# Kernel optimization log

Measured on AMD Instinct MI355X. Metric: run time of the kernel, lower is better.

The kernel has to match this reference:

```python
import jax, jax.numpy as jnp
import numpy as np

B, N, M = 2, 4096, 4096
QUERY_DIM = 1024
CONTEXT_DIM = 1024
HEADS = 16
DIM_HEAD = 64
INNER = HEADS * DIM_HEAD


def setup_inputs() -> dict:
    key = jax.random.key(0)
    ks = jax.random.split(key, 7)
    s = 0.02
    return {
        "x": jax.random.normal(ks[0], (B, N, QUERY_DIM), dtype=jnp.float32),
        "context": jax.random.normal(ks[1], (B, M, CONTEXT_DIM), dtype=jnp.float32),
        "Wq": jax.random.normal(ks[2], (QUERY_DIM, INNER), dtype=jnp.float32) * s,
        "Wk": jax.random.normal(ks[3], (CONTEXT_DIM, INNER), dtype=jnp.float32) * s,
        "Wv": jax.random.normal(ks[4], (CONTEXT_DIM, INNER), dtype=jnp.float32) * s,
        "Wo": jax.random.normal(ks[5], (INNER, QUERY_DIM), dtype=jnp.float32) * s,
        "bo": jnp.zeros((QUERY_DIM,), dtype=jnp.float32),
    }


def reference(x, context, Wq, Wk, Wv, Wo, bo):
    scale = DIM_HEAD ** -0.5
    # projections, then split heads: b n (h d) -> b h n d
    q = (x @ Wq).reshape(B, N, HEADS, DIM_HEAD).transpose(0, 2, 1, 3)
    k = (context @ Wk).reshape(B, M, HEADS, DIM_HEAD).transpose(0, 2, 1, 3)
    v = (context @ Wv).reshape(B, M, HEADS, DIM_HEAD).transpose(0, 2, 1, 3)
    attn = jnp.einsum('bhnd,bhmd->bhnm', q, k) * scale  # [B,H,N,M]
    attn = jax.nn.softmax(attn, axis=-1)
    out = jnp.einsum('bhnm,bhmd->bhnd', attn, v)
    out = out.transpose(0, 2, 1, 3).reshape(B, N, INNER)  # b h n d -> b n (h d)
    return out @ Wo + bo  # dropout(p=0) is identity
```

## Files before the change

kernel.cpp:

```cpp
#include <hip/hip_runtime.h>

using f16    = _Float16;
using f16x2  = __attribute__((ext_vector_type(2))) _Float16;
using f16x4  = __attribute__((ext_vector_type(4))) _Float16;
using f16x8  = __attribute__((ext_vector_type(8))) _Float16;
using h16x2  = __attribute__((ext_vector_type(2))) __fp16;
using f32x4  = __attribute__((ext_vector_type(4))) float;
using f32x16 = __attribute__((ext_vector_type(16))) float;
using u32    = unsigned int;
using u32x4  = __attribute__((ext_vector_type(4))) u32;

#define DI __device__ __forceinline__

DI f16x4 pack4(float a, float b, float c, float d) {
  f16x2 lo = __builtin_bit_cast(f16x2, __builtin_amdgcn_cvt_pkrtz(a, b));
  f16x2 hi = __builtin_bit_cast(f16x2, __builtin_amdgcn_cvt_pkrtz(c, d));
  f16x4 r; r[0] = lo[0]; r[1] = lo[1]; r[2] = hi[0]; r[3] = hi[1];
  return r;
}

DI u32 pk32(float a, float b) {
  return __builtin_bit_cast(u32, __builtin_amdgcn_cvt_pkrtz(a, b));
}

DI float dot1(u32 wrd, float acc) {
#if __has_builtin(__builtin_amdgcn_fdot2)
  h16x2 one; one[0] = (__fp16)1.f; one[1] = (__fp16)1.f;
  return __builtin_amdgcn_fdot2(__builtin_bit_cast(h16x2, wrd), one, acc, false);
#else
  f16x2 p = __builtin_bit_cast(f16x2, wrd);
  return acc + (float)p[0] + (float)p[1];
#endif
}

DI void gll16(const void* g, void* l) {
  __builtin_amdgcn_global_load_lds((const __attribute__((address_space(1))) u32*)g,
                                   (__attribute__((address_space(3))) u32*)l, 16, 0, 0);
}

DI f16x8 ldfrag(const void* base, int row, int u4) {
  int phys = u4 ^ (row & 7);
  return *(const f16x8*)((const char*)base + row * 128 + phys * 16);
}

DI f32x4 mfma16(f16x8 a, f16x8 b, f32x4 c) {
  return __builtin_amdgcn_mfma_f32_16x16x32_f16(a, b, c, 0, 0, 0);
}
DI f32x16 mfma32(f16x8 a, f16x8 b, f32x16 c) {
  return __builtin_amdgcn_mfma_f32_32x32x16_f16(a, b, c, 0, 0, 0);
}

__global__ void k_cvt2(const float* __restrict__ x, const float* __restrict__ ctx,
                       f16* __restrict__ dst, int n4) {
  int z = blockIdx.y;
  const float* s = z ? ctx : x;
  f16* d = dst + (size_t)z * 8192 * 1024;
  int i = blockIdx.x * blockDim.x + threadIdx.x;
  if (i < n4) {
    float4 v = ((const float4*)s)[i];
    ((f16x4*)d)[i] = pack4(v.x, v.y, v.z, v.w);
  }
}

__global__ void k_wt4(const float* __restrict__ Wq, const float* __restrict__ Wk,
                      const float* __restrict__ Wv, const float* __restrict__ Wo,
                      f16* __restrict__ WTb) {
  int z = blockIdx.z;
  const float* W = z == 0 ? Wq : z == 1 ? Wk : z == 2 ? Wv : Wo;
  f16* WT = WTb + (size_t)z * 1024 * 1024;
  __shared__ float tile[64][65];
  int k0 = blockIdx.y * 64, n0 = blockIdx.x * 64;
  int t = threadIdx.x;
#pragma unroll
  for (int p = 0; p < 4; ++p) {
    int r = p * 16 + (t >> 4);
    int c = (t & 15) * 4;
    float4 v = *(const float4*)&W[(size_t)(k0 + r) * 1024 + n0 + c];
    tile[r][c] = v.x; tile[r][c + 1] = v.y; tile[r][c + 2] = v.z; tile[r][c + 3] = v.w;
  }
  __syncthreads();
#pragma unroll
  for (int p = 0; p < 4; ++p) {
    int n = p * 16 + (t >> 4);
    int k = (t & 15) * 4;
    *(f16x4*)&WT[(size_t)(n0 + n) * 1024 + k0 + k] =
        pack4(tile[k][n], tile[k + 1][n], tile[k + 2][n], tile[k + 3][n]);
  }
}

template <int EPI>
__global__ __launch_bounds__(256) void k_gemm(const f16* __restrict__ A, const f16* __restrict__ Bt,
                                              void* __restrict__ Cp, const float* __restrict__ bias) {
  __shared__ __align__(16) char smem[65536];
  f16* sA = (f16*)smem;
  f16* sB = (f16*)(smem + 32768);
  const int tid = threadIdx.x, w = tid >> 6, lane = tid & 63;
  const int g = lane >> 4, l15 = lane & 15, l7 = lane & 7, l8 = lane >> 3;
  const int m0 = blockIdx.x * 128, n0 = blockIdx.y * 128;
  const int wm = w >> 1, wn = w & 1;
  const int uswz = l7 ^ l8;

  auto stage = [&](int kt, int bufi) {
    int kb = kt * 128;
#pragma unroll
    for (int q = 0; q < 4; ++q) {
      int row = w * 32 + q * 8 + l8;
      gll16((const char*)A + (size_t)(m0 + row) * 2048 + kb + uswz * 16,
            (char*)sA + bufi * 16384 + (w * 32 + q * 8) * 128);
      gll16((const char*)Bt + (size_t)(n0 + row) * 2048 + kb + uswz * 16,
            (char*)sB + bufi * 16384 + (w * 32 + q * 8) * 128);
    }
  };

  f32x4 acc[4][4] = {};
  stage(0, 0);
  for (int kt = 0; kt < 16; ++kt) {
    asm volatile("s_waitcnt vmcnt(0)" ::: "memory");
    __syncthreads();
    if (kt + 1 < 16) stage(kt + 1, (kt + 1) & 1);
    const f16* aL = (const f16*)((const char*)sA + (kt & 1) * 16384);
    const f16* bL = (const f16*)((const char*)sB + (kt & 1) * 16384);
#pragma unroll
    for (int kc = 0; kc < 2; ++kc) {
      f16x8 af[4], bf[4];
#pragma unroll
      for (int mi = 0; mi < 4; ++mi) af[mi] = ldfrag(aL, wm * 64 + mi * 16 + l15, kc * 4 + g);
#pragma unroll
      for (int ni = 0; ni < 4; ++ni) bf[ni] = ldfrag(bL, wn * 64 + ni * 16 + l15, kc * 4 + g);
#pragma unroll
      for (int mi = 0; mi < 4; ++mi)
#pragma unroll
        for (int ni = 0; ni < 4; ++ni) acc[mi][ni] = mfma16(af[mi], bf[ni], acc[mi][ni]);
    }
  }

  if (EPI == 2) {
    float* C = (float*)Cp;
    float bv[4];
#pragma unroll
    for (int ni = 0; ni < 4; ++ni) bv[ni] = bias[n0 + wn * 64 + ni * 16 + l15];
#pragma unroll
    for (int mi = 0; mi < 4; ++mi)
#pragma unroll
      for (int ni = 0; ni < 4; ++ni) {
        int col = n0 + wn * 64 + ni * 16 + l15;
#pragma unroll
        for (int i = 0; i < 4; ++i) {
          int row = m0 + wm * 64 + mi * 16 + g * 4 + i;
          C[(size_t)row * 1024 + col] = acc[mi][ni][i] + bv[ni];
        }
      }
    return;
  }

  __syncthreads();
  f16* Ct = (f16*)smem;
  if (EPI == 0) {
#pragma unroll
    for (int mi = 0; mi < 4; ++mi)
#pragma unroll
      for (int ni = 0; ni < 4; ++ni) {
        int col = wn * 64 + ni * 16 + l15;
#pragma unroll
        for (int i = 0; i < 4; ++i) Ct[(wm * 64 + mi * 16 + g * 4 + i) * 136 + col] = (f16)acc[mi][ni][i];
      }
    __syncthreads();
    f16* C = (f16*)Cp;
#pragma unroll
    for (int p = 0; p < 8; ++p) {
      int r = p * 16 + (tid >> 4), cu = tid & 15;
      f16x8 v = *(const f16x8*)((const char*)Ct + r * 272 + cu * 16);
      *(f16x8*)((char*)C + (size_t)(m0 + r) * 2048 + n0 * 2 + cu * 16) = v;
    }
  } else {
#pragma unroll
    for (int mi = 0; mi < 4; ++mi)
#pragma unroll
      for (int ni = 0; ni < 4; ++ni) {
        int n = wn * 64 + ni * 16 + l15;
        int mcol = wm * 64 + mi * 16 + g * 4;
        *(f16x4*)&Ct[n * 136 + mcol] =
            pack4(acc[mi][ni][0], acc[mi][ni][1], acc[mi][ni][2], acc[mi][ni][3]);
      }
    __syncthreads();
    int b = m0 >> 12, mm = m0 & 4095;
    f16* V = (f16*)Cp;
#pragma unroll
    for (int p = 0; p < 8; ++p) {
      int n = p * 16 + (tid >> 4), cu = tid & 15;
      f16x8 v = *(const f16x8*)((const char*)Ct + n * 272 + cu * 16);
      *(f16x8*)((char*)V + ((size_t)(b * 1024 + n0 + n) * 4096 + mm) * 2 + cu * 16) = v;
    }
  }
}

__global__ __launch_bounds__(256, 2) void k_attn(const f16* __restrict__ Qh, const f16* __restrict__ Kh,
                                                 const f16* __restrict__ VT, f16* __restrict__ Oh) {
  __shared__ __align__(16) char smem[32768];
  const int tid = threadIdx.x, w = tid >> 6, lane = tid & 63;
  const int hi = lane >> 5, c = lane & 31, l7 = lane & 7, l8 = lane >> 3;
  const int bid = blockIdx.x;
  const int bh = (bid & 7) * 4 + (bid >> 7);
  const int qc = (bid >> 3) & 15;
  const int b = bh >> 4, h = bh & 15;
  const int rowB = b * 4096;
  const int qrow0 = rowB + qc * 256 + w * 64;
  const int uswz = l7 ^ l8;

  const f16 ce = (f16)0.18033688f;
  f16x8 bQ0[4], bQ1[4];
#pragma unroll
  for (int ks = 0; ks < 4; ++ks) {
    f16x8 r0 = *(const f16x8*)(Qh + (size_t)(qrow0 + c) * 1024 + h * 64 + ks * 16 + hi * 8);
    f16x8 r1 = *(const f16x8*)(Qh + (size_t)(qrow0 + 32 + c) * 1024 + h * 64 + ks * 16 + hi * 8);
#pragma unroll
    for (int e = 0; e < 8; ++e) { r0[e] *= ce; r1[e] *= ce; }
    bQ0[ks] = r0; bQ1[ks] = r1;
  }

  const f32x16 Z = {};
  f32x16 acc00 = {}, acc01 = {}, acc10 = {}, acc11 = {};
  float lrow0 = 0.f, lrow1 = 0.f;

  auto stage = [&](int t, int bufi) {
    int r = w * 16 + l8;
#pragma unroll
    for (int q = 0; q < 2; ++q) {
      gll16((const char*)Kh + ((size_t)(rowB + t * 64 + r + q * 8) * 1024 + h * 64) * 2 + uswz * 16,
            (char*)smem + bufi * 8192 + (w * 16 + q * 8) * 128);
      gll16((const char*)VT + ((size_t)(b * 1024 + h * 64 + r + q * 8) * 4096 + t * 64) * 2 + uswz * 16,
            (char*)smem + 16384 + bufi * 8192 + (w * 16 + q * 8) * 128);
    }
  };

  auto softpack = [&](f32x16 sA, f32x16 sB, f16x8* bp) -> float {
#pragma unroll
    for (int i = 0; i < 16; ++i) sA[i] = __builtin_amdgcn_exp2f(sA[i]);
#pragma unroll
    for (int i = 0; i < 16; ++i) sB[i] = __builtin_amdgcn_exp2f(sB[i]);
    u32 a[8], d[8];
#pragma unroll
    for (int i = 0; i < 8; ++i) a[i] = pk32(sA[2 * i], sA[2 * i + 1]);
#pragma unroll
    for (int i = 0; i < 8; ++i) d[i] = pk32(sB[2 * i], sB[2 * i + 1]);
    float s0 = 0.f, s1 = 0.f;
#pragma unroll
    for (int i = 0; i < 8; ++i) s0 = dot1(a[i], s0);
#pragma unroll
    for (int i = 0; i < 8; ++i) s1 = dot1(d[i], s1);
    {
      auto s02 = __builtin_amdgcn_permlane32_swap(a[0], a[2], false, false);
      auto s13 = __builtin_amdgcn_permlane32_swap(a[1], a[3], false, false);
      auto s46 = __builtin_amdgcn_permlane32_swap(a[4], a[6], false, false);
      auto s57 = __builtin_amdgcn_permlane32_swap(a[5], a[7], false, false);
      u32x4 w0 = {s02[0], s13[0], s02[1], s13[1]};
      u32x4 w1 = {s46[0], s57[0], s46[1], s57[1]};
      bp[0] = __builtin_bit_cast(f16x8, w0);
      bp[1] = __builtin_bit_cast(f16x8, w1);
    }
    {
      auto s02 = __builtin_amdgcn_permlane32_swap(d[0], d[2], false, false);
      auto s13 = __builtin_amdgcn_permlane32_swap(d[1], d[3], false, false);
      auto s46 = __builtin_amdgcn_permlane32_swap(d[4], d[6], false, false);
      auto s57 = __builtin_amdgcn_permlane32_swap(d[5], d[7], false, false);
      u32x4 w0 = {s02[0], s13[0], s02[1], s13[1]};
      u32x4 w1 = {s46[0], s57[0], s46[1], s57[1]};
      bp[2] = __builtin_bit_cast(f16x8, w0);
      bp[3] = __builtin_bit_cast(f16x8, w1);
    }
    return s0 + s1;
  };

  stage(0, 0);
  for (int t = 0; t < 64; ++t) {
    asm volatile("s_waitcnt vmcnt(0)" ::: "memory");
    __syncthreads();
    if (t + 1 < 64) stage(t + 1, (t + 1) & 1);
    const char* Kl = (const char*)smem + (t & 1) * 8192;
    const char* Vl = (const char*)smem + 16384 + (t & 1) * 8192;

    __builtin_amdgcn_s_setprio(1);
    f16x8 a0 = ldfrag(Kl, c, hi), a1 = ldfrag(Kl, 32 + c, hi);
    f32x16 st00 = mfma32(a0, bQ0[0], Z);
    f32x16 st01 = mfma32(a0, bQ1[0], Z);
    f32x16 st10 = mfma32(a1, bQ0[0], Z);
    f32x16 st11 = mfma32(a1, bQ1[0], Z);
#pragma unroll
    for (int ks = 1; ks < 4; ++ks) {
      a0 = ldfrag(Kl, c, ks * 2 + hi); a1 = ldfrag(Kl, 32 + c, ks * 2 + hi);
      st00 = mfma32(a0, bQ0[ks], st00);
      st01 = mfma32(a0, bQ1[ks], st01);
      st10 = mfma32(a1, bQ0[ks], st10);
      st11 = mfma32(a1, bQ1[ks], st11);
    }
    __builtin_amdgcn_s_setprio(0);

    f16x8 bpA[4], bpB[4];
    lrow0 += softpack(st00, st10, bpA);
    lrow1 += softpack(st01, st11, bpB);

    __builtin_amdgcn_s_setprio(1);
#pragma unroll
    for (int ks = 0; ks < 4; ++ks) {
      f16x8 av0 = ldfrag(Vl, c, ks * 2 + hi);
      f16x8 av1 = ldfrag(Vl, 32 + c, ks * 2 + hi);
      acc00 = mfma32(av0, bpA[ks], acc00);
      acc01 = mfma32(av0, bpB[ks], acc01);
      acc10 = mfma32(av1, bpA[ks], acc10);
      acc11 = mfma32(av1, bpB[ks], acc11);
    }
    __builtin_amdgcn_s_setprio(0);
  }

  float inv0, inv1;
  {
    auto r2 = __builtin_amdgcn_permlane32_swap(__builtin_bit_cast(u32, lrow0),
                                               __builtin_bit_cast(u32, lrow0), false, false);
    inv0 = 1.0f / (__builtin_bit_cast(float, r2[0]) + __builtin_bit_cast(float, r2[1]));
  }
  {
    auto r2 = __builtin_amdgcn_permlane32_swap(__builtin_bit_cast(u32, lrow1),
                                               __builtin_bit_cast(u32, lrow1), false, false);
    inv1 = 1.0f / (__builtin_bit_cast(float, r2[0]) + __builtin_bit_cast(float, r2[1]));
  }

  __syncthreads();
  char* myO = (char*)smem + w * 8192;
#pragma unroll
  for (int rb = 0; rb < 2; ++rb) {
    float iv = rb ? inv1 : inv0;
    int r = rb * 32 + c;
#pragma unroll
    for (int dt = 0; dt < 2; ++dt) {
      const f32x16& A = rb ? (dt ? acc11 : acc01) : (dt ? acc10 : acc00);
#pragma unroll
      for (int q8 = 0; q8 < 4; ++q8) {
        f16x4 hv = pack4(A[q8 * 4] * iv, A[q8 * 4 + 1] * iv, A[q8 * 4 + 2] * iv, A[q8 * 4 + 3] * iv);
        int slot = dt * 4 + q8;
        *(f16x4*)(myO + r * 128 + ((slot ^ (r & 7)) * 16) + hi * 8) = hv;
      }
    }
  }
#pragma unroll
  for (int p = 0; p < 8; ++p) {
    int r = p * 8 + l8;
    f16x8 v = *(const f16x8*)(myO + r * 128 + ((l7 ^ (r & 7)) * 16));
    *(f16x8*)((char*)Oh + ((size_t)(qrow0 + r) * 1024 + h * 64) * 2 + l7 * 16) = v;
  }
}

extern "C" void kernel_launch(void* const* d_in, const int* in_sizes, int n_in,
                              void* d_out, int out_size, void* d_ws, size_t ws_size,
                              hipStream_t stream) {
  const float* x   = (const float*)d_in[0];
  const float* ctx = (const float*)d_in[1];
  const float* Wq  = (const float*)d_in[2];
  const float* Wk  = (const float*)d_in[3];
  const float* Wv  = (const float*)d_in[4];
  const float* Wo  = (const float*)d_in[5];
  const float* bo  = (const float*)d_in[6];
  float* out = (float*)d_out;

  const size_t NR = 8192, KD = 1024;
  if (ws_size < (size_t)(5 * NR * KD * 2 + 4 * KD * KD * 2)) return;

  char* ws = (char*)d_ws;
  f16* xh  = (f16*)ws;
  f16* ch  = xh + NR * KD;
  f16* WqT = ch + NR * KD;
  f16* WkT = WqT + KD * KD;
  f16* WvT = WkT + KD * KD;
  f16* WoT = WvT + KD * KD;
  f16* Qh  = WoT + KD * KD;
  f16* Kh  = Qh + NR * KD;
  f16* VT  = Kh + NR * KD;
  f16* Oh  = xh;

  int n4 = (int)(NR * KD / 4);
  k_cvt2<<<dim3((n4 + 255) / 256, 2), dim3(256), 0, stream>>>(x, ctx, xh, n4);
  k_wt4<<<dim3(16, 16, 4), dim3(256), 0, stream>>>(Wq, Wk, Wv, Wo, WqT);

  dim3 gg(64, 8), gb(256);
  k_gemm<0><<<gg, gb, 0, stream>>>(xh, WqT, (void*)Qh, nullptr);
  k_gemm<0><<<gg, gb, 0, stream>>>(ch, WkT, (void*)Kh, nullptr);
  k_gemm<1><<<gg, gb, 0, stream>>>(ch, WvT, (void*)VT, nullptr);

  k_attn<<<dim3(512), dim3(256), 0, stream>>>(Qh, Kh, VT, Oh);

  k_gemm<2><<<gg, gb, 0, stream>>>(Oh, WoT, (void*)out, bo);
}
```

Measured before the change: 272.4 us.

## Pre-tile K/V into fragment-major layout and shrink attention blocks to two waves

```diff
diff --git a/kernel.cpp b/kernel.cpp
--- a/kernel.cpp
+++ b/kernel.cpp
@@ -41,6 +41,10 @@
 DI f16x8 ldfrag(const void* base, int row, int u4) {
   int phys = u4 ^ (row & 7);
   return *(const f16x8*)((const char*)base + row * 128 + phys * 16);
+}
+
+DI f16x8 ldsc(const void* base, int row, int slot) {
+  return *(const f16x8*)((const char*)base + slot * 1024 + row * 16);
 }
 
 DI f32x4 mfma16(f16x8 a, f16x8 b, f32x4 c) {
@@ -155,7 +159,7 @@
 
   __syncthreads();
   f16* Ct = (f16*)smem;
-  if (EPI == 0) {
+  if (EPI == 0 || EPI == 3) {
 #pragma unroll
     for (int mi = 0; mi < 4; ++mi)
 #pragma unroll
@@ -165,12 +169,25 @@
         for (int i = 0; i < 4; ++i) Ct[(wm * 64 + mi * 16 + g * 4 + i) * 136 + col] = (f16)acc[mi][ni][i];
       }
     __syncthreads();
-    f16* C = (f16*)Cp;
-#pragma unroll
-    for (int p = 0; p < 8; ++p) {
-      int r = p * 16 + (tid >> 4), cu = tid & 15;
-      f16x8 v = *(const f16x8*)((const char*)Ct + r * 272 + cu * 16);
-      *(f16x8*)((char*)C + (size_t)(m0 + r) * 2048 + n0 * 2 + cu * 16) = v;
+    if (EPI == 0) {
+      f16* C = (f16*)Cp;
+#pragma unroll
+      for (int p = 0; p < 8; ++p) {
+        int r = p * 16 + (tid >> 4), cu = tid & 15;
+        f16x8 v = *(const f16x8*)((const char*)Ct + r * 272 + cu * 16);
+        *(f16x8*)((char*)C + (size_t)(m0 + r) * 2048 + n0 * 2 + cu * 16) = v;
+      }
+    } else {
+      int b = m0 >> 12, mmr = m0 & 4095;
+#pragma unroll
+      for (int p = 0; p < 8; ++p) {
+        int r = p * 16 + (tid >> 4), cu = tid & 15;
+        f16x8 v = *(const f16x8*)((const char*)Ct + r * 272 + cu * 16);
+        int kvr = mmr + r;
+        int h = (n0 >> 6) + (cu >> 3);
+        size_t off = ((size_t)((b * 16 + h) * 64 + (kvr >> 6))) * 8192 + (cu & 7) * 1024 + (kvr & 63) * 16;
+        *(f16x8*)((char*)Cp + off) = v;
+      }
     }
   } else {
 #pragma unroll
@@ -184,28 +201,29 @@
       }
     __syncthreads();
     int b = m0 >> 12, mm = m0 & 4095;
-    f16* V = (f16*)Cp;
 #pragma unroll
     for (int p = 0; p < 8; ++p) {
-      int n = p * 16 + (tid >> 4), cu = tid & 15;
-      f16x8 v = *(const f16x8*)((const char*)Ct + n * 272 + cu * 16);
-      *(f16x8*)((char*)V + ((size_t)(b * 1024 + n0 + n) * 4096 + mm) * 2 + cu * 16) = v;
-    }
-  }
-}
-
-__global__ __launch_bounds__(256, 2) void k_attn(const f16* __restrict__ Qh, const f16* __restrict__ Kh,
-                                                 const f16* __restrict__ VT, f16* __restrict__ Oh) {
+      int r = p * 16 + (tid >> 4), cu = tid & 15;
+      f16x8 v = *(const f16x8*)((const char*)Ct + r * 272 + cu * 16);
+      int h = (n0 + r) >> 6, d = (n0 + r) & 63;
+      size_t off = ((size_t)((b * 16 + h) * 64 + (mm >> 6) + (cu >> 3))) * 8192 + (cu & 7) * 1024 + d * 16;
+      *(f16x8*)((char*)Cp + off) = v;
+    }
+  }
+}
+
+__global__ __launch_bounds__(128, 4) void k_attn(const f16* __restrict__ Qh, const f16* __restrict__ Ks,
+                                                 const f16* __restrict__ Vs, f16* __restrict__ Oh) {
   __shared__ __align__(16) char smem[32768];
   const int tid = threadIdx.x, w = tid >> 6, lane = tid & 63;
   const int hi = lane >> 5, c = lane & 31, l7 = lane & 7, l8 = lane >> 3;
   const int bid = blockIdx.x;
-  const int bh = (bid & 7) * 4 + (bid >> 7);
-  const int qc = (bid >> 3) & 15;
+  const int bh = (bid & 7) * 4 + (bid >> 8);
+  const int qc = (bid >> 3) & 31;
   const int b = bh >> 4, h = bh & 15;
   const int rowB = b * 4096;
-  const int qrow0 = rowB + qc * 256 + w * 64;
-  const int uswz = l7 ^ l8;
+  const int qrow0 = rowB + qc * 128 + w * 64;
+  const size_t tb = (size_t)bh * 64 * 8192;
 
   const f16 ce = (f16)0.18033688f;
   f16x8 bQ0[4], bQ1[4];
@@ -223,13 +241,13 @@
   float lrow0 = 0.f, lrow1 = 0.f;
 
   auto stage = [&](int t, int bufi) {
-    int r = w * 16 + l8;
-#pragma unroll
-    for (int q = 0; q < 2; ++q) {
-      gll16((const char*)Kh + ((size_t)(rowB + t * 64 + r + q * 8) * 1024 + h * 64) * 2 + uswz * 16,
-            (char*)smem + bufi * 8192 + (w * 16 + q * 8) * 128);
-      gll16((const char*)VT + ((size_t)(b * 1024 + h * 64 + r + q * 8) * 4096 + t * 64) * 2 + uswz * 16,
-            (char*)smem + 16384 + bufi * 8192 + (w * 16 + q * 8) * 128);
+    const char* bK = (const char*)Ks + tb + (size_t)t * 8192 + lane * 16;
+    const char* bV = (const char*)Vs + tb + (size_t)t * 8192 + lane * 16;
+#pragma unroll
+    for (int q = 0; q < 4; ++q) {
+      int slot = w * 4 + q;
+      gll16(bK + slot * 1024, (char*)smem + bufi * 8192 + slot * 1024);
+      gll16(bV + slot * 1024, (char*)smem + 16384 + bufi * 8192 + slot * 1024);
     }
   };
 
@@ -280,14 +298,14 @@
     const char* Vl = (const char*)smem + 16384 + (t & 1) * 8192;
 
     __builtin_amdgcn_s_setprio(1);
-    f16x8 a0 = ldfrag(Kl, c, hi), a1 = ldfrag(Kl, 32 + c, hi);
+    f16x8 a0 = ldsc(Kl, c, hi), a1 = ldsc(Kl, 32 + c, hi);
     f32x16 st00 = mfma32(a0, bQ0[0], Z);
     f32x16 st01 = mfma32(a0, bQ1[0], Z);
     f32x16 st10 = mfma32(a1, bQ0[0], Z);
     f32x16 st11 = mfma32(a1, bQ1[0], Z);
 #pragma unroll
     for (int ks = 1; ks < 4; ++ks) {
-      a0 = ldfrag(Kl, c, ks * 2 + hi); a1 = ldfrag(Kl, 32 + c, ks * 2 + hi);
+      a0 = ldsc(Kl, c, ks * 2 + hi); a1 = ldsc(Kl, 32 + c, ks * 2 + hi);
       st00 = mfma32(a0, bQ0[ks], st00);
       st01 = mfma32(a0, bQ1[ks], st01);
       st10 = mfma32(a1, bQ0[ks], st10);
@@ -302,8 +320,8 @@
     __builtin_amdgcn_s_setprio(1);
 #pragma unroll
     for (int ks = 0; ks < 4; ++ks) {
-      f16x8 av0 = ldfrag(Vl, c, ks * 2 + hi);
-      f16x8 av1 = ldfrag(Vl, 32 + c, ks * 2 + hi);
+      f16x8 av0 = ldsc(Vl, c, ks * 2 + hi);
+      f16x8 av1 = ldsc(Vl, 32 + c, ks * 2 + hi);
       acc00 = mfma32(av0, bpA[ks], acc00);
       acc01 = mfma32(av0, bpB[ks], acc01);
       acc10 = mfma32(av1, bpA[ks], acc10);
@@ -372,8 +390,8 @@
   f16* WvT = WkT + KD * KD;
   f16* WoT = WvT + KD * KD;
   f16* Qh  = WoT + KD * KD;
-  f16* Kh  = Qh + NR * KD;
-  f16* VT  = Kh + NR * KD;
+  f16* Ks  = Qh + NR * KD;
+  f16* Vs  = Ks + NR * KD;
   f16* Oh  = xh;
 
   int n4 = (int)(NR * KD / 4);
@@ -382,10 +400,10 @@
 
   dim3 gg(64, 8), gb(256);
   k_gemm<0><<<gg, gb, 0, stream>>>(xh, WqT, (void*)Qh, nullptr);
-  k_gemm<0><<<gg, gb, 0, stream>>>(ch, WkT, (void*)Kh, nullptr);
-  k_gemm<1><<<gg, gb, 0, stream>>>(ch, WvT, (void*)VT, nullptr);
-
-  k_attn<<<dim3(512), dim3(256), 0, stream>>>(Qh, Kh, VT, Oh);
+  k_gemm<3><<<gg, gb, 0, stream>>>(ch, WkT, (void*)Ks, nullptr);
+  k_gemm<1><<<gg, gb, 0, stream>>>(ch, WvT, (void*)Vs, nullptr);
+
+  k_attn<<<dim3(1024), dim3(128), 0, stream>>>(Qh, Ks, Vs, Oh);
 
   k_gemm<2><<<gg, gb, 0, stream>>>(Oh, WoT, (void*)out, bo);
 }
```

Measured after the change: 341.8 us, median of 5. 1.25x slower.
